# Performance work log

Hardware: AMD Instinct MI355X
Metric: run time of the kernel (lower is better)

## Reference

```python
import jax, jax.numpy as jnp
import numpy as np

N, D = 8192, 256
ALPHA, BETA, K = 50.0, 1.0, 2


def setup_inputs() -> dict:
    key = jax.random.key(0)
    k1, k2, k3, k4 = jax.random.split(key, 4)
    Q = jax.random.normal(k1, (N, D), dtype=jnp.float32)
    # 0/1 similarity structure; diagonal forced nonzero so no row is fully masked
    sim = jax.random.randint(k2, (N, N), 0, 2).astype(jnp.float32)
    sim = sim.at[jnp.arange(N), jnp.arange(N)].set(1.0)
    # nn.Linear(in_dim, in_dim) params: y = x @ W.T + b
    bound = 1.0 / np.sqrt(D)
    W = jax.random.uniform(k3, (D, D), jnp.float32, -bound, bound)
    b = jax.random.uniform(k4, (D,), jnp.float32, -bound, bound)
    return {"Q": Q, "sim_mat": sim, "W": W, "b": b}


def reference(Q, sim_mat, W, b):
    mask = sim_mat == 0  # (N, N) bool, constant across iterations
    H = Q
    for _ in range(K):
        H_proj = H @ W.T + b                      # (N, d)
        scores = H_proj @ H_proj.T                # (N, N)
        scores = jnp.where(mask, -jnp.inf, scores)
        lamb = jax.nn.softmax(scores, axis=1)     # (N, N)
        numerator = ALPHA * Q + BETA * (lamb @ H)
        denominator = ALPHA + BETA * jnp.sum(lamb, axis=1, keepdims=True)
        H = numerator / denominator
    return H
```

## Files before the change

### kernel.cpp

```cpp
#include <hip/hip_runtime.h>
#include <hip/hip_bf16.h>

#define NN 8192
#define DD 256
#define ALPHA 50.0f
#define BETA 1.0f
#define THR 10.0f
#define KQ 8
#define KEYS (NN / KQ)
#define KTILE 64
#define ITERS (KEYS / KTILE)
#define QROWS 128

typedef __attribute__((ext_vector_type(8))) short short8;
typedef __attribute__((ext_vector_type(4))) float f32x4;

static __device__ __forceinline__ ushort f2bf(float f) {
    union { __hip_bfloat16 h; ushort u; } v;
    v.h = __float2bfloat16(f);
    return v.u;
}
static __device__ __forceinline__ float bf2f(ushort u) {
    union { unsigned u; float f; } v; v.u = ((unsigned)u) << 16;
    return v.f;
}
static __device__ __forceinline__ void gl_lds16(const void* g, void* l) {
    __builtin_amdgcn_global_load_lds(
        (const __attribute__((address_space(1))) unsigned int*)g,
        (__attribute__((address_space(3))) unsigned int*)l, 16, 0, 0);
}

__global__ void k_wconv(const float* __restrict__ W, ushort* __restrict__ Wb) {
    int i = blockIdx.x * 256 + threadIdx.x;
    Wb[i] = f2bf(W[i]);
}

__global__ __launch_bounds__(256) void k_pack(const float* __restrict__ sim,
                                              unsigned* __restrict__ bits) {
    __shared__ unsigned char nibs[256];
    int row = blockIdx.x;
    int tid = threadIdx.x;
    for (int p = 0; p < 8; ++p) {
        int col = p * 1024 + tid * 4;
        float4 v = *reinterpret_cast<const float4*>(sim + (size_t)row * NN + col);
        unsigned char nib = (unsigned char)((v.x != 0.f) | ((v.y != 0.f) << 1) |
                                            ((v.z != 0.f) << 2) | ((v.w != 0.f) << 3));
        nibs[tid] = nib;
        __syncthreads();
        if (tid < 32) {
            unsigned word = 0;
#pragma unroll
            for (int i = 0; i < 8; ++i) word |= ((unsigned)nibs[tid * 8 + i]) << (4 * i);
            bits[row * (NN / 32) + p * 32 + tid] = word;
        }
        __syncthreads();
    }
}

__global__ __launch_bounds__(256) void k_convert(const float* __restrict__ H,
                                                 ushort* __restrict__ Hv,
                                                 ushort* __restrict__ Hvt) {
    __shared__ ushort T[64][72];
    int tile = blockIdx.x;
    int r0 = (tile >> 2) * 64;
    int c0 = (tile & 3) * 64;
    int tid = threadIdx.x;
    int tr = tid >> 4;
    int tc = (tid & 15) * 4;
    for (int i = 0; i < 4; ++i) {
        int r = tr + i * 16;
        float4 v = *reinterpret_cast<const float4*>(H + (size_t)(r0 + r) * DD + c0 + tc);
        ushort4 o;
        o.x = f2bf(v.x); o.y = f2bf(v.y); o.z = f2bf(v.z); o.w = f2bf(v.w);
        *reinterpret_cast<ushort4*>(Hv + (size_t)(r0 + r) * DD + c0 + tc) = o;
        T[tc + 0][r] = o.x; T[tc + 1][r] = o.y; T[tc + 2][r] = o.z; T[tc + 3][r] = o.w;
    }
    __syncthreads();
    for (int i = 0; i < 4; ++i) {
        int c = tr + i * 16;
        ushort4 o;
        o.x = T[c][tc + 0]; o.y = T[c][tc + 1]; o.z = T[c][tc + 2]; o.w = T[c][tc + 3];
        *reinterpret_cast<ushort4*>(Hvt + (size_t)(c0 + c) * NN + r0 + tc) = o;
    }
}

__global__ __launch_bounds__(256) void k_proj(const ushort* __restrict__ Hv,
                                              const ushort* __restrict__ Wb,
                                              const float* __restrict__ b,
                                              ushort* __restrict__ Hp) {
    int w = threadIdx.x >> 6;
    int lane = threadIdx.x & 63;
    int row0 = (blockIdx.x >> 1) * 64 + w * 16;
    int ch = blockIdx.x & 1;
    int lr = lane & 15;
    int lk = lane >> 4;
    short8 af[8];
    for (int kk = 0; kk < 8; ++kk)
        af[kk] = *reinterpret_cast<const short8*>(Hv + (size_t)(row0 + lr) * DD + kk * 32 + lk * 8);
    for (int t = 0; t < 8; ++t) {
        f32x4 acc = {0.f, 0.f, 0.f, 0.f};
        int col = (ch * 8 + t) * 16 + lr;
        for (int kk = 0; kk < 8; ++kk) {
            short8 bf = *reinterpret_cast<const short8*>(Wb + (size_t)col * DD + kk * 32 + lk * 8);
            acc = __builtin_amdgcn_mfma_f32_16x16x32_bf16(af[kk], bf, acc, 0, 0, 0);
        }
        float bias = b[col];
        for (int j = 0; j < 4; ++j) {
            int row = row0 + lk * 4 + j;
            Hp[(size_t)row * DD + col] = f2bf(acc[j] + bias);
        }
    }
}

#define PSTR 40
#define KBYTES (KTILE * 256 * 2)
#define VBYTES (256 * KTILE * 2)
#define PBYTES (8 * 16 * PSTR * 2)
#define BBYTES (QROWS * 32 * 4)
#define SMEM_ATTN (2 * KBYTES + 2 * VBYTES + PBYTES + BBYTES)
__global__ __launch_bounds__(512) void k_attn(const ushort* __restrict__ Hp,
                                              const ushort* __restrict__ Hvt,
                                              const unsigned* __restrict__ bits,
                                              ushort* __restrict__ Opart,
                                              float* __restrict__ mpart,
                                              float* __restrict__ lpart) {
    extern __shared__ char smem[];
    ushort* KlB = (ushort*)smem;
    ushort* VlB = (ushort*)(smem + 2 * KBYTES);
    ushort* Pl  = (ushort*)(smem + 2 * KBYTES + 2 * VBYTES);
    unsigned* Bl = (unsigned*)(smem + 2 * KBYTES + 2 * VBYTES + PBYTES);

    const int tid = threadIdx.x;
    const int w = tid >> 6;
    const int lane = tid & 63;
    const int lr = lane & 15;
    const int lk = lane >> 4;
    const int bid = blockIdx.x;
    const int kq = bid & 7;
    const int qt = bid >> 3;
    const int rw0 = qt * QROWS + w * 16;
    const int kstart = kq * KEYS;

    int kSrc[4], vSrc[4], dstO[4];
#pragma unroll
    for (int i = 0; i < 4; ++i) {
        int S = i * 512 + tid;
        int rK = S >> 5, cpK = S & 31;
        kSrc[i] = rK * 256 + (cpK ^ (rK & 7)) * 8;
        int rV = S >> 3, cpV = S & 7;
        vSrc[i] = rV * NN + (cpV ^ (rV & 7)) * 8;
        dstO[i] = S * 8;
    }
    auto stageK = [&](int buf, int kb) {
        const ushort* Kg = Hp + (size_t)kb * DD;
        ushort* base = KlB + buf * (KTILE * 256);
#pragma unroll
        for (int i = 0; i < 4; ++i) gl_lds16(Kg + kSrc[i], base + dstO[i]);
    };
    auto stageV = [&](int buf, int kb) {
        const ushort* Vg = Hvt + kb;
        ushort* base = VlB + buf * (256 * KTILE);
#pragma unroll
        for (int i = 0; i < 4; ++i) gl_lds16(Vg + vSrc[i], base + dstO[i]);
    };

    int Koff[8];
#pragma unroll
    for (int kk = 0; kk < 8; ++kk)
        Koff[kk] = (lr << 9) + ((((kk << 2) + lk) ^ (lr & 7)) << 4);
    const int vBaseA = (lr << 7) + ((lk ^ (lr & 7)) << 4);
    const int vBaseB = (lr << 7) + (((4 + lk) ^ (lr & 7)) << 4);

    short8 qf[8];
#pragma unroll
    for (int kk = 0; kk < 8; ++kk)
        qf[kk] = *reinterpret_cast<const short8*>(Hp + (size_t)(rw0 + lr) * DD + kk * 32 + lk * 8);

    f32x4 o[17];
#pragma unroll
    for (int t = 0; t < 17; ++t) o[t] = {0.f, 0.f, 0.f, 0.f};
    float m[4] = {-1e30f, -1e30f, -1e30f, -1e30f};

    short8 ones;
#pragma unroll
    for (int e = 0; e < 8; ++e) ones[e] = (short)0x3f80;

    {
        const unsigned* Bg = bits + (size_t)(qt * QROWS) * (NN / 32) + kq * 32;
#pragma unroll
        for (int i = 0; i < 2; ++i) {
            int S = i * 512 + tid;
            int r = S >> 3, c = S & 7;
            gl_lds16(Bg + (size_t)r * (NN / 32) + c * 4, Bl + S * 4);
        }
    }
    stageK(0, kstart);
    stageV(0, kstart);
    asm volatile("s_waitcnt vmcnt(0)" ::: "memory");
    __builtin_amdgcn_s_barrier();
    __builtin_amdgcn_sched_barrier(0);

    ushort* Pw = Pl + (size_t)w * 16 * PSTR;
    const int mrow = (w * 16 + lk * 4) * 32;
    int cur = 0;
    for (int it = 0; it < ITERS; ++it) {
        const int kb = kstart + it * KTILE;
        const bool staged = (it + 1 < ITERS);
        if (staged) {
            stageK(cur ^ 1, kb + KTILE);
            stageV(cur ^ 1, kb + KTILE);
        }
        unsigned mwa[4], mwb[4];
#pragma unroll
        for (int j = 0; j < 4; ++j) {
            mwa[j] = Bl[mrow + j * 32 + it * 2];
            mwb[j] = Bl[mrow + j * 32 + it * 2 + 1];
        }

        const char* Kb = (const char*)(KlB + cur * (KTILE * 256));
        f32x4 s0a = {0.f,0.f,0.f,0.f}, s1a = {0.f,0.f,0.f,0.f};
        f32x4 s0b = {0.f,0.f,0.f,0.f}, s1b = {0.f,0.f,0.f,0.f};
        __builtin_amdgcn_s_setprio(1);
#pragma unroll
        for (int kk = 0; kk < 8; ++kk) {
            short8 k0a = *reinterpret_cast<const short8*>(Kb + Koff[kk]);
            short8 k1a = *reinterpret_cast<const short8*>(Kb + Koff[kk] + (16 << 9));
            short8 k0b = *reinterpret_cast<const short8*>(Kb + Koff[kk] + (32 << 9));
            short8 k1b = *reinterpret_cast<const short8*>(Kb + Koff[kk] + (48 << 9));
            s0a = __builtin_amdgcn_mfma_f32_16x16x32_bf16(qf[kk], k0a, s0a, 0, 0, 0);
            s1a = __builtin_amdgcn_mfma_f32_16x16x32_bf16(qf[kk], k1a, s1a, 0, 0, 0);
            s0b = __builtin_amdgcn_mfma_f32_16x16x32_bf16(qf[kk], k0b, s0b, 0, 0, 0);
            s1b = __builtin_amdgcn_mfma_f32_16x16x32_bf16(qf[kk], k1b, s1b, 0, 0, 0);
        }
        __builtin_amdgcn_s_setprio(0);

        const char* Vb = (const char*)(VlB + cur * (256 * KTILE));
        {
            float c = -1e30f;
#pragma unroll
            for (int j = 0; j < 4; ++j) {
                float a0 = ((mwa[j] >> lr) & 1u) ? s0a[j] : -1e30f;
                float a1 = ((mwa[j] >> (lr + 16)) & 1u) ? s1a[j] : -1e30f;
                s0a[j] = a0; s1a[j] = a1;
                c = fmaxf(c, fmaxf(a0, a1) - m[j]);
            }
            if (__any(c > THR)) {
#pragma unroll
                for (int j = 0; j < 4; ++j) {
                    float mx = fmaxf(s0a[j], s1a[j]);
                    mx = fmaxf(mx, __shfl_xor(mx, 1));
                    mx = fmaxf(mx, __shfl_xor(mx, 2));
                    mx = fmaxf(mx, __shfl_xor(mx, 4));
                    mx = fmaxf(mx, __shfl_xor(mx, 8));
                    float mn = fmaxf(m[j], mx);
                    float scale = __expf(m[j] - mn);
                    m[j] = mn;
#pragma unroll
                    for (int t = 0; t < 17; ++t) o[t][j] *= scale;
                }
            }
#pragma unroll
            for (int j = 0; j < 4; ++j) {
                Pw[(lk * 4 + j) * PSTR + lr]      = f2bf(__expf(s0a[j] - m[j]));
                Pw[(lk * 4 + j) * PSTR + 16 + lr] = f2bf(__expf(s1a[j] - m[j]));
            }
            asm volatile("s_waitcnt lgkmcnt(0)" ::: "memory");
            __builtin_amdgcn_sched_barrier(0);
            short8 pa = *reinterpret_cast<const short8*>(Pw + lr * PSTR + lk * 8);
            __builtin_amdgcn_s_setprio(1);
#pragma unroll
            for (int t = 0; t < 16; ++t) {
                short8 vf = *reinterpret_cast<const short8*>(Vb + vBaseA + (t << 11));
                o[t] = __builtin_amdgcn_mfma_f32_16x16x32_bf16(pa, vf, o[t], 0, 0, 0);
            }
            o[16] = __builtin_amdgcn_mfma_f32_16x16x32_bf16(pa, ones, o[16], 0, 0, 0);
            __builtin_amdgcn_s_setprio(0);
        }
        {
            float c = -1e30f;
#pragma unroll
            for (int j = 0; j < 4; ++j) {
                float a0 = ((mwb[j] >> lr) & 1u) ? s0b[j] : -1e30f;
                float a1 = ((mwb[j] >> (lr + 16)) & 1u) ? s1b[j] : -1e30f;
                s0b[j] = a0; s1b[j] = a1;
                c = fmaxf(c, fmaxf(a0, a1) - m[j]);
            }
            if (__any(c > THR)) {
#pragma unroll
                for (int j = 0; j < 4; ++j) {
                    float mx = fmaxf(s0b[j], s1b[j]);
                    mx = fmaxf(mx, __shfl_xor(mx, 1));
                    mx = fmaxf(mx, __shfl_xor(mx, 2));
                    mx = fmaxf(mx, __shfl_xor(mx, 4));
                    mx = fmaxf(mx, __shfl_xor(mx, 8));
                    float mn = fmaxf(m[j], mx);
                    float scale = __expf(m[j] - mn);
                    m[j] = mn;
#pragma unroll
                    for (int t = 0; t < 17; ++t) o[t][j] *= scale;
                }
            }
#pragma unroll
            for (int j = 0; j < 4; ++j) {
                Pw[(lk * 4 + j) * PSTR + lr]      = f2bf(__expf(s0b[j] - m[j]));
                Pw[(lk * 4 + j) * PSTR + 16 + lr] = f2bf(__expf(s1b[j] - m[j]));
            }
            asm volatile("s_waitcnt lgkmcnt(0)" ::: "memory");
            __builtin_amdgcn_sched_barrier(0);
            short8 pb = *reinterpret_cast<const short8*>(Pw + lr * PSTR + lk * 8);
            __builtin_amdgcn_s_setprio(1);
#pragma unroll
            for (int t = 0; t < 16; ++t) {
                short8 vf = *reinterpret_cast<const short8*>(Vb + vBaseB + (t << 11));
                o[t] = __builtin_amdgcn_mfma_f32_16x16x32_bf16(pb, vf, o[t], 0, 0, 0);
            }
            o[16] = __builtin_amdgcn_mfma_f32_16x16x32_bf16(pb, ones, o[16], 0, 0, 0);
            __builtin_amdgcn_s_setprio(0);
        }
        if (staged) {
            asm volatile("s_waitcnt vmcnt(0)" ::: "memory");
            __builtin_amdgcn_s_barrier();
            __builtin_amdgcn_sched_barrier(0);
        }
        cur ^= 1;
    }

    ushort* op = Opart + ((size_t)kq * NN + rw0) * DD;
#pragma unroll
    for (int t = 0; t < 16; ++t)
#pragma unroll
        for (int j = 0; j < 4; ++j)
            op[(size_t)(lk * 4 + j) * DD + t * 16 + lr] = f2bf(o[t][j]);
    if (lr == 0) {
#pragma unroll
        for (int j = 0; j < 4; ++j) {
            mpart[kq * NN + rw0 + lk * 4 + j] = m[j];
            lpart[kq * NN + rw0 + lk * 4 + j] = o[16][j];
        }
    }
}

__global__ __launch_bounds__(256) void k_merge8(const ushort* __restrict__ Opart,
                                                const float* __restrict__ mpart,
                                                const float* __restrict__ lpart,
                                                const float* __restrict__ Qo,
                                                float* __restrict__ dst) {
    int w = threadIdx.x >> 6;
    int lane = threadIdx.x & 63;
    int r0 = blockIdx.x * 32 + w * 8;
    for (int rr = 0; rr < 8; ++rr) {
        int r = r0 + rr;
        float mv[8], f[8];
        float M = -1e30f;
#pragma unroll
        for (int p = 0; p < 8; ++p) { mv[p] = mpart[p * NN + r]; M = fmaxf(M, mv[p]); }
        float L = 0.f;
#pragma unroll
        for (int p = 0; p < 8; ++p) { f[p] = __expf(mv[p] - M); L += f[p] * lpart[p * NN + r]; }
        float invL = 1.0f / L;
        int c = lane * 4;
        float a0 = 0.f, a1 = 0.f, a2 = 0.f, a3 = 0.f;
#pragma unroll
        for (int p = 0; p < 8; ++p) {
            ushort4 u = *reinterpret_cast<const ushort4*>(Opart + ((size_t)p * NN + r) * DD + c);
            a0 += f[p] * bf2f(u.x); a1 += f[p] * bf2f(u.y);
            a2 += f[p] * bf2f(u.z); a3 += f[p] * bf2f(u.w);
        }
        float4 qv = *reinterpret_cast<const float4*>(Qo + (size_t)r * DD + c);
        float4 ov;
        ov.x = (ALPHA * qv.x + a0 * invL) * (1.0f / (ALPHA + BETA));
        ov.y = (ALPHA * qv.y + a1 * invL) * (1.0f / (ALPHA + BETA));
        ov.z = (ALPHA * qv.z + a2 * invL) * (1.0f / (ALPHA + BETA));
        ov.w = (ALPHA * qv.w + a3 * invL) * (1.0f / (ALPHA + BETA));
        *reinterpret_cast<float4*>(dst + (size_t)r * DD + c) = ov;
    }
}

extern "C" void kernel_launch(void* const* d_in, const int* in_sizes, int n_in,
                              void* d_out, int out_size, void* d_ws, size_t ws_size,
                              hipStream_t stream) {
    const float* Q   = (const float*)d_in[0];
    const float* sim = (const float*)d_in[1];
    const float* W   = (const float*)d_in[2];
    const float* b   = (const float*)d_in[3];
    float* out = (float*)d_out;

    char* ws = (char*)d_ws;
    size_t off = 0;
    ushort* Hv   = (ushort*)(ws + off); off += (size_t)NN * DD * 2;
    ushort* HvtA = (ushort*)(ws + off); off += (size_t)NN * DD * 2;
    ushort* HvtB = (ushort*)(ws + off); off += (size_t)NN * DD * 2;
    ushort* Hp   = (ushort*)(ws + off); off += (size_t)NN * DD * 2;
    ushort* Wb   = (ushort*)(ws + off); off += (size_t)DD * DD * 2;
    unsigned* bits = (unsigned*)(ws + off); off += (size_t)NN * (NN / 32) * 4;
    float*  H1   = (float*)(ws + off);  off += (size_t)NN * DD * 4;
    ushort* Opart = (ushort*)(ws + off); off += (size_t)KQ * NN * DD * 2;
    float*  mpart = (float*)(ws + off);  off += (size_t)KQ * NN * 4;
    float*  lpart = (float*)(ws + off);  off += (size_t)KQ * NN * 4;

    (void)hipFuncSetAttribute((const void*)k_attn,
                              hipFuncAttributeMaxDynamicSharedMemorySize, SMEM_ATTN);

    k_wconv<<<DD * DD / 256, 256, 0, stream>>>(W, Wb);
    k_pack<<<NN, 256, 0, stream>>>(sim, bits);
    k_convert<<<(NN / 64) * (DD / 64), 256, 0, stream>>>(Q, Hv, HvtA);

    k_proj<<<NN / 32, 256, 0, stream>>>(Hv, Wb, b, Hp);
    k_attn<<<(NN / QROWS) * KQ, 512, SMEM_ATTN, stream>>>(Hp, HvtA, bits, Opart, mpart, lpart);
    k_merge8<<<NN / 32, 256, 0, stream>>>(Opart, mpart, lpart, Q, H1);
    k_convert<<<(NN / 64) * (DD / 64), 256, 0, stream>>>(H1, Hv, HvtB);

    k_proj<<<NN / 32, 256, 0, stream>>>(Hv, Wb, b, Hp);
    k_attn<<<(NN / QROWS) * KQ, 512, SMEM_ATTN, stream>>>(Hp, HvtB, bits, Opart, mpart, lpart);
    k_merge8<<<NN / 32, 256, 0, stream>>>(Opart, mpart, lpart, Q, out);
}
```

Baseline: 330.5 us.

## Replace double-buffered K/V staging with single buffer and direct mask reads

Removes the double-buffered K/V LDS staging and the LDS copy of the mask bitwords. Each iteration now finishes its compute, hits a barrier, loads the next K/V tile and waits for it, and mask bits are read straight from global memory. This cuts LDS use, which could let more blocks fit per CU, but it gives up overlap between loads and MFMA work and adds a barrier per iteration.

```diff
diff --git a/kernel.cpp b/kernel.cpp
--- a/kernel.cpp
+++ b/kernel.cpp
@@ -116,8 +116,7 @@
 #define KBYTES (KTILE * 256 * 2)
 #define VBYTES (256 * KTILE * 2)
 #define PBYTES (8 * 16 * PSTR * 2)
-#define BBYTES (QROWS * 32 * 4)
-#define SMEM_ATTN (2 * KBYTES + 2 * VBYTES + PBYTES + BBYTES)
+#define SMEM_ATTN (KBYTES + VBYTES + PBYTES)
 __global__ __launch_bounds__(512) void k_attn(const ushort* __restrict__ Hp,
                                               const ushort* __restrict__ Hvt,
                                               const unsigned* __restrict__ bits,
@@ -125,10 +124,9 @@
                                               float* __restrict__ mpart,
                                               float* __restrict__ lpart) {
     extern __shared__ char smem[];
-    ushort* KlB = (ushort*)smem;
-    ushort* VlB = (ushort*)(smem + 2 * KBYTES);
-    ushort* Pl  = (ushort*)(smem + 2 * KBYTES + 2 * VBYTES);
-    unsigned* Bl = (unsigned*)(smem + 2 * KBYTES + 2 * VBYTES + PBYTES);
+    ushort* Kl = (ushort*)smem;
+    ushort* Vl = (ushort*)(smem + KBYTES);
+    ushort* Pl = (ushort*)(smem + KBYTES + VBYTES);
 
     const int tid = threadIdx.x;
     const int w = tid >> 6;
@@ -151,17 +149,15 @@
         vSrc[i] = rV * NN + (cpV ^ (rV & 7)) * 8;
         dstO[i] = S * 8;
     }
-    auto stageK = [&](int buf, int kb) {
+    auto stageK = [&](int kb) {
         const ushort* Kg = Hp + (size_t)kb * DD;
-        ushort* base = KlB + buf * (KTILE * 256);
-#pragma unroll
-        for (int i = 0; i < 4; ++i) gl_lds16(Kg + kSrc[i], base + dstO[i]);
+#pragma unroll
+        for (int i = 0; i < 4; ++i) gl_lds16(Kg + kSrc[i], Kl + dstO[i]);
     };
-    auto stageV = [&](int buf, int kb) {
+    auto stageV = [&](int kb) {
         const ushort* Vg = Hvt + kb;
-        ushort* base = VlB + buf * (256 * KTILE);
-#pragma unroll
-        for (int i = 0; i < 4; ++i) gl_lds16(Vg + vSrc[i], base + dstO[i]);
+#pragma unroll
+        for (int i = 0; i < 4; ++i) gl_lds16(Vg + vSrc[i], Vl + dstO[i]);
     };
 
     int Koff[8];
@@ -185,39 +181,25 @@
 #pragma unroll
     for (int e = 0; e < 8; ++e) ones[e] = (short)0x3f80;
 
-    {
-        const unsigned* Bg = bits + (size_t)(qt * QROWS) * (NN / 32) + kq * 32;
-#pragma unroll
-        for (int i = 0; i < 2; ++i) {
-            int S = i * 512 + tid;
-            int r = S >> 3, c = S & 7;
-            gl_lds16(Bg + (size_t)r * (NN / 32) + c * 4, Bl + S * 4);
-        }
-    }
-    stageK(0, kstart);
-    stageV(0, kstart);
+    stageK(kstart);
+    stageV(kstart);
     asm volatile("s_waitcnt vmcnt(0)" ::: "memory");
     __builtin_amdgcn_s_barrier();
     __builtin_amdgcn_sched_barrier(0);
 
     ushort* Pw = Pl + (size_t)w * 16 * PSTR;
-    const int mrow = (w * 16 + lk * 4) * 32;
-    int cur = 0;
+    const int rowbase = (rw0 + lk * 4) * (NN / 32);
     for (int it = 0; it < ITERS; ++it) {
         const int kb = kstart + it * KTILE;
-        const bool staged = (it + 1 < ITERS);
-        if (staged) {
-            stageK(cur ^ 1, kb + KTILE);
-            stageV(cur ^ 1, kb + KTILE);
-        }
+        const int wi = kb >> 5;
         unsigned mwa[4], mwb[4];
 #pragma unroll
         for (int j = 0; j < 4; ++j) {
-            mwa[j] = Bl[mrow + j * 32 + it * 2];
-            mwb[j] = Bl[mrow + j * 32 + it * 2 + 1];
-        }
-
-        const char* Kb = (const char*)(KlB + cur * (KTILE * 256));
+            mwa[j] = bits[rowbase + j * (NN / 32) + wi];
+            mwb[j] = bits[rowbase + j * (NN / 32) + wi + 1];
+        }
+
+        const char* Kb = (const char*)Kl;
         f32x4 s0a = {0.f,0.f,0.f,0.f}, s1a = {0.f,0.f,0.f,0.f};
         f32x4 s0b = {0.f,0.f,0.f,0.f}, s1b = {0.f,0.f,0.f,0.f};
         __builtin_amdgcn_s_setprio(1);
@@ -234,7 +216,7 @@
         }
         __builtin_amdgcn_s_setprio(0);
 
-        const char* Vb = (const char*)(VlB + cur * (256 * KTILE));
+        const char* Vb = (const char*)Vl;
         {
             float c = -1e30f;
 #pragma unroll
@@ -317,12 +299,15 @@
             o[16] = __builtin_amdgcn_mfma_f32_16x16x32_bf16(pb, ones, o[16], 0, 0, 0);
             __builtin_amdgcn_s_setprio(0);
         }
-        if (staged) {
+        if (it + 1 < ITERS) {
+            __builtin_amdgcn_s_barrier();
+            __builtin_amdgcn_sched_barrier(0);
+            stageK(kb + KTILE);
+            stageV(kb + KTILE);
             asm volatile("s_waitcnt vmcnt(0)" ::: "memory");
             __builtin_amdgcn_s_barrier();
             __builtin_amdgcn_sched_barrier(0);
         }
-        cur ^= 1;
     }
 
     ushort* op = Opart + ((size_t)kq * NN + rw0) * DD;
```

Measured after the change: 342.1 us. +3.5%, slower.

## Process two 16-row query tiles per wave to reuse K/V LDS fragments

Applied to the files above, without the earlier changes.

Each wave now handles 32 query rows (two 16-row sub-tiles) instead of 16, doubling the block's query tile to 256 rows. Every K and V fragment read from LDS feeds two MFMAs, halving LDS read traffic per unit of work and halving how often K/V tiles are staged from global memory. The mask bitmap is no longer preloaded into LDS and is read directly from global memory each iteration. In exchange, register pressure roughly doubles (two sets of 17 accumulators plus Q fragments), which risks spilling or lower occupancy, and the grid now has half as many blocks.

```diff
diff --git a/kernel.cpp b/kernel.cpp
--- a/kernel.cpp
+++ b/kernel.cpp
@@ -10,7 +10,7 @@
 #define KEYS (NN / KQ)
 #define KTILE 64
 #define ITERS (KEYS / KTILE)
-#define QROWS 128
+#define QROWS 256
 
 typedef __attribute__((ext_vector_type(8))) short short8;
 typedef __attribute__((ext_vector_type(4))) float f32x4;
@@ -115,9 +115,8 @@
 #define PSTR 40
 #define KBYTES (KTILE * 256 * 2)
 #define VBYTES (256 * KTILE * 2)
-#define PBYTES (8 * 16 * PSTR * 2)
-#define BBYTES (QROWS * 32 * 4)
-#define SMEM_ATTN (2 * KBYTES + 2 * VBYTES + PBYTES + BBYTES)
+#define PBYTES (8 * 2 * 16 * PSTR * 2)
+#define SMEM_ATTN (2 * KBYTES + 2 * VBYTES + PBYTES)
 __global__ __launch_bounds__(512) void k_attn(const ushort* __restrict__ Hp,
                                               const ushort* __restrict__ Hvt,
                                               const unsigned* __restrict__ bits,
@@ -128,7 +127,6 @@
     ushort* KlB = (ushort*)smem;
     ushort* VlB = (ushort*)(smem + 2 * KBYTES);
     ushort* Pl  = (ushort*)(smem + 2 * KBYTES + 2 * VBYTES);
-    unsigned* Bl = (unsigned*)(smem + 2 * KBYTES + 2 * VBYTES + PBYTES);
 
     const int tid = threadIdx.x;
     const int w = tid >> 6;
@@ -138,7 +136,7 @@
     const int bid = blockIdx.x;
     const int kq = bid & 7;
     const int qt = bid >> 3;
-    const int rw0 = qt * QROWS + w * 16;
+    const int rw0 = qt * QROWS + w * 32;
     const int kstart = kq * KEYS;
 
     int kSrc[4], vSrc[4], dstO[4];
@@ -171,55 +169,55 @@
     const int vBaseA = (lr << 7) + ((lk ^ (lr & 7)) << 4);
     const int vBaseB = (lr << 7) + (((4 + lk) ^ (lr & 7)) << 4);
 
-    short8 qf[8];
-#pragma unroll
-    for (int kk = 0; kk < 8; ++kk)
-        qf[kk] = *reinterpret_cast<const short8*>(Hp + (size_t)(rw0 + lr) * DD + kk * 32 + lk * 8);
-
-    f32x4 o[17];
-#pragma unroll
-    for (int t = 0; t < 17; ++t) o[t] = {0.f, 0.f, 0.f, 0.f};
-    float m[4] = {-1e30f, -1e30f, -1e30f, -1e30f};
+    short8 qfA[8], qfB[8];
+#pragma unroll
+    for (int kk = 0; kk < 8; ++kk) {
+        qfA[kk] = *reinterpret_cast<const short8*>(Hp + (size_t)(rw0 + lr) * DD + kk * 32 + lk * 8);
+        qfB[kk] = *reinterpret_cast<const short8*>(Hp + (size_t)(rw0 + 16 + lr) * DD + kk * 32 + lk * 8);
+    }
+
+    f32x4 oA[17], oB[17];
+#pragma unroll
+    for (int t = 0; t < 17; ++t) { oA[t] = {0.f,0.f,0.f,0.f}; oB[t] = {0.f,0.f,0.f,0.f}; }
+    float mA[4] = {-1e30f, -1e30f, -1e30f, -1e30f};
+    float mB[4] = {-1e30f, -1e30f, -1e30f, -1e30f};
 
     short8 ones;
 #pragma unroll
     for (int e = 0; e < 8; ++e) ones[e] = (short)0x3f80;
 
-    {
-        const unsigned* Bg = bits + (size_t)(qt * QROWS) * (NN / 32) + kq * 32;
-#pragma unroll
-        for (int i = 0; i < 2; ++i) {
-            int S = i * 512 + tid;
-            int r = S >> 3, c = S & 7;
-            gl_lds16(Bg + (size_t)r * (NN / 32) + c * 4, Bl + S * 4);
-        }
-    }
     stageK(0, kstart);
     stageV(0, kstart);
     asm volatile("s_waitcnt vmcnt(0)" ::: "memory");
     __builtin_amdgcn_s_barrier();
     __builtin_amdgcn_sched_barrier(0);
 
-    ushort* Pw = Pl + (size_t)w * 16 * PSTR;
-    const int mrow = (w * 16 + lk * 4) * 32;
+    ushort* PwA = Pl + (size_t)(w * 2) * 16 * PSTR;
+    ushort* PwB = PwA + 16 * PSTR;
+    const int rbA = (rw0 + lk * 4) * (NN / 32);
+    const int rbB = rbA + 16 * (NN / 32);
     int cur = 0;
     for (int it = 0; it < ITERS; ++it) {
         const int kb = kstart + it * KTILE;
-        const bool staged = (it + 1 < ITERS);
-        if (staged) {
+        if (it + 1 < ITERS) {
             stageK(cur ^ 1, kb + KTILE);
             stageV(cur ^ 1, kb + KTILE);
         }
-        unsigned mwa[4], mwb[4];
+        const int wi = kb >> 5;
+        unsigned mAa[4], mAb[4], mBa[4], mBb[4];
 #pragma unroll
         for (int j = 0; j < 4; ++j) {
-            mwa[j] = Bl[mrow + j * 32 + it * 2];
-            mwb[j] = Bl[mrow + j * 32 + it * 2 + 1];
+            mAa[j] = bits[rbA + j * (NN / 32) + wi];
+            mAb[j] = bits[rbA + j * (NN / 32) + wi + 1];
+            mBa[j] = bits[rbB + j * (NN / 32) + wi];
+            mBb[j] = bits[rbB + j * (NN / 32) + wi + 1];
         }
 
         const char* Kb = (const char*)(KlB + cur * (KTILE * 256));
-        f32x4 s0a = {0.f,0.f,0.f,0.f}, s1a = {0.f,0.f,0.f,0.f};
-        f32x4 s0b = {0.f,0.f,0.f,0.f}, s1b = {0.f,0.f,0.f,0.f};
+        f32x4 sA0a = {0.f,0.f,0.f,0.f}, sA1a = {0.f,0.f,0.f,0.f};
+        f32x4 sA0b = {0.f,0.f,0.f,0.f}, sA1b = {0.f,0.f,0.f,0.f};
+        f32x4 sB0a = {0.f,0.f,0.f,0.f}, sB1a = {0.f,0.f,0.f,0.f};
+        f32x4 sB0b = {0.f,0.f,0.f,0.f}, sB1b = {0.f,0.f,0.f,0.f};
         __builtin_amdgcn_s_setprio(1);
 #pragma unroll
         for (int kk = 0; kk < 8; ++kk) {
@@ -227,10 +225,14 @@
             short8 k1a = *reinterpret_cast<const short8*>(Kb + Koff[kk] + (16 << 9));
             short8 k0b = *reinterpret_cast<const short8*>(Kb + Koff[kk] + (32 << 9));
             short8 k1b = *reinterpret_cast<const short8*>(Kb + Koff[kk] + (48 << 9));
-            s0a = __builtin_amdgcn_mfma_f32_16x16x32_bf16(qf[kk], k0a, s0a, 0, 0, 0);
-            s1a = __builtin_amdgcn_mfma_f32_16x16x32_bf16(qf[kk], k1a, s1a, 0, 0, 0);
-            s0b = __builtin_amdgcn_mfma_f32_16x16x32_bf16(qf[kk], k0b, s0b, 0, 0, 0);
-            s1b = __builtin_amdgcn_mfma_f32_16x16x32_bf16(qf[kk], k1b, s1b, 0, 0, 0);
+            sA0a = __builtin_amdgcn_mfma_f32_16x16x32_bf16(qfA[kk], k0a, sA0a, 0, 0, 0);
+            sB0a = __builtin_amdgcn_mfma_f32_16x16x32_bf16(qfB[kk], k0a, sB0a, 0, 0, 0);
+            sA1a = __builtin_amdgcn_mfma_f32_16x16x32_bf16(qfA[kk], k1a, sA1a, 0, 0, 0);
+            sB1a = __builtin_amdgcn_mfma_f32_16x16x32_bf16(qfB[kk], k1a, sB1a, 0, 0, 0);
+            sA0b = __builtin_amdgcn_mfma_f32_16x16x32_bf16(qfA[kk], k0b, sA0b, 0, 0, 0);
+            sB0b = __builtin_amdgcn_mfma_f32_16x16x32_bf16(qfB[kk], k0b, sB0b, 0, 0, 0);
+            sA1b = __builtin_amdgcn_mfma_f32_16x16x32_bf16(qfA[kk], k1b, sA1b, 0, 0, 0);
+            sB1b = __builtin_amdgcn_mfma_f32_16x16x32_bf16(qfB[kk], k1b, sB1b, 0, 0, 0);
         }
         __builtin_amdgcn_s_setprio(0);
 
@@ -239,85 +241,123 @@
             float c = -1e30f;
 #pragma unroll
             for (int j = 0; j < 4; ++j) {
-                float a0 = ((mwa[j] >> lr) & 1u) ? s0a[j] : -1e30f;
-                float a1 = ((mwa[j] >> (lr + 16)) & 1u) ? s1a[j] : -1e30f;
-                s0a[j] = a0; s1a[j] = a1;
-                c = fmaxf(c, fmaxf(a0, a1) - m[j]);
+                float x0 = ((mAa[j] >> lr) & 1u) ? sA0a[j] : -1e30f;
+                float x1 = ((mAa[j] >> (lr + 16)) & 1u) ? sA1a[j] : -1e30f;
+                sA0a[j] = x0; sA1a[j] = x1;
+                c = fmaxf(c, fmaxf(x0, x1) - mA[j]);
+                float y0 = ((mBa[j] >> lr) & 1u) ? sB0a[j] : -1e30f;
+                float y1 = ((mBa[j] >> (lr + 16)) & 1u) ? sB1a[j] : -1e30f;
+                sB0a[j] = y0; sB1a[j] = y1;
+                c = fmaxf(c, fmaxf(y0, y1) - mB[j]);
             }
             if (__any(c > THR)) {
 #pragma unroll
                 for (int j = 0; j < 4; ++j) {
-                    float mx = fmaxf(s0a[j], s1a[j]);
+                    float mx = fmaxf(sA0a[j], sA1a[j]);
                     mx = fmaxf(mx, __shfl_xor(mx, 1));
                     mx = fmaxf(mx, __shfl_xor(mx, 2));
                     mx = fmaxf(mx, __shfl_xor(mx, 4));
                     mx = fmaxf(mx, __shfl_xor(mx, 8));
-                    float mn = fmaxf(m[j], mx);
-                    float scale = __expf(m[j] - mn);
-                    m[j] = mn;
-#pragma unroll
-                    for (int t = 0; t < 17; ++t) o[t][j] *= scale;
+                    float mn = fmaxf(mA[j], mx);
+                    float sc = __expf(mA[j] - mn);
+                    mA[j] = mn;
+#pragma unroll
+                    for (int t = 0; t < 17; ++t) oA[t][j] *= sc;
+                    float my = fmaxf(sB0a[j], sB1a[j]);
+                    my = fmaxf(my, __shfl_xor(my, 1));
+                    my = fmaxf(my, __shfl_xor(my, 2));
+                    my = fmaxf(my, __shfl_xor(my, 4));
+                    my = fmaxf(my, __shfl_xor(my, 8));
+                    float mn2 = fmaxf(mB[j], my);
+                    float sc2 = __expf(mB[j] - mn2);
+                    mB[j] = mn2;
+#pragma unroll
+                    for (int t = 0; t < 17; ++t) oB[t][j] *= sc2;
                 }
             }
 #pragma unroll
             for (int j = 0; j < 4; ++j) {
-                Pw[(lk * 4 + j) * PSTR + lr]      = f2bf(__expf(s0a[j] - m[j]));
-                Pw[(lk * 4 + j) * PSTR + 16 + lr] = f2bf(__expf(s1a[j] - m[j]));
+                PwA[(lk * 4 + j) * PSTR + lr]      = f2bf(__expf(sA0a[j] - mA[j]));
+                PwA[(lk * 4 + j) * PSTR + 16 + lr] = f2bf(__expf(sA1a[j] - mA[j]));
+                PwB[(lk * 4 + j) * PSTR + lr]      = f2bf(__expf(sB0a[j] - mB[j]));
+                PwB[(lk * 4 + j) * PSTR + 16 + lr] = f2bf(__expf(sB1a[j] - mB[j]));
             }
             asm volatile("s_waitcnt lgkmcnt(0)" ::: "memory");
             __builtin_amdgcn_sched_barrier(0);
-            short8 pa = *reinterpret_cast<const short8*>(Pw + lr * PSTR + lk * 8);
+            short8 paA = *reinterpret_cast<const short8*>(PwA + lr * PSTR + lk * 8);
+            short8 paB = *reinterpret_cast<const short8*>(PwB + lr * PSTR + lk * 8);
             __builtin_amdgcn_s_setprio(1);
 #pragma unroll
             for (int t = 0; t < 16; ++t) {
                 short8 vf = *reinterpret_cast<const short8*>(Vb + vBaseA + (t << 11));
-                o[t] = __builtin_amdgcn_mfma_f32_16x16x32_bf16(pa, vf, o[t], 0, 0, 0);
-            }
-            o[16] = __builtin_amdgcn_mfma_f32_16x16x32_bf16(pa, ones, o[16], 0, 0, 0);
+                oA[t] = __builtin_amdgcn_mfma_f32_16x16x32_bf16(paA, vf, oA[t], 0, 0, 0);
+                oB[t] = __builtin_amdgcn_mfma_f32_16x16x32_bf16(paB, vf, oB[t], 0, 0, 0);
+            }
+            oA[16] = __builtin_amdgcn_mfma_f32_16x16x32_bf16(paA, ones, oA[16], 0, 0, 0);
+            oB[16] = __builtin_amdgcn_mfma_f32_16x16x32_bf16(paB, ones, oB[16], 0, 0, 0);
             __builtin_amdgcn_s_setprio(0);
         }
         {
             float c = -1e30f;
 #pragma unroll
             for (int j = 0; j < 4; ++j) {
-                float a0 = ((mwb[j] >> lr) & 1u) ? s0b[j] : -1e30f;
-                float a1 = ((mwb[j] >> (lr + 16)) & 1u) ? s1b[j] : -1e30f;
-                s0b[j] = a0; s1b[j] = a1;
-                c = fmaxf(c, fmaxf(a0, a1) - m[j]);
+                float x0 = ((mAb[j] >> lr) & 1u) ? sA0b[j] : -1e30f;
+                float x1 = ((mAb[j] >> (lr + 16)) & 1u) ? sA1b[j] : -1e30f;
+                sA0b[j] = x0; sA1b[j] = x1;
+                c = fmaxf(c, fmaxf(x0, x1) - mA[j]);
+                float y0 = ((mBb[j] >> lr) & 1u) ? sB0b[j] : -1e30f;
+                float y1 = ((mBb[j] >> (lr + 16)) & 1u) ? sB1b[j] : -1e30f;
+                sB0b[j] = y0; sB1b[j] = y1;
+                c = fmaxf(c, fmaxf(y0, y1) - mB[j]);
             }
             if (__any(c > THR)) {
 #pragma unroll
                 for (int j = 0; j < 4; ++j) {
-                    float mx = fmaxf(s0b[j], s1b[j]);
+                    float mx = fmaxf(sA0b[j], sA1b[j]);
                     mx = fmaxf(mx, __shfl_xor(mx, 1));
                     mx = fmaxf(mx, __shfl_xor(mx, 2));
                     mx = fmaxf(mx, __shfl_xor(mx, 4));
                     mx = fmaxf(mx, __shfl_xor(mx, 8));
-                    float mn = fmaxf(m[j], mx);
-                    float scale = __expf(m[j] - mn);
-                    m[j] = mn;
-#pragma unroll
-                    for (int t = 0; t < 17; ++t) o[t][j] *= scale;
+                    float mn = fmaxf(mA[j], mx);
+                    float sc = __expf(mA[j] - mn);
+                    mA[j] = mn;
+#pragma unroll
+                    for (int t = 0; t < 17; ++t) oA[t][j] *= sc;
+                    float my = fmaxf(sB0b[j], sB1b[j]);
+                    my = fmaxf(my, __shfl_xor(my, 1));
+                    my = fmaxf(my, __shfl_xor(my, 2));
+                    my = fmaxf(my, __shfl_xor(my, 4));
+                    my = fmaxf(my, __shfl_xor(my, 8));
+                    float mn2 = fmaxf(mB[j], my);
+                    float sc2 = __expf(mB[j] - mn2);
+                    mB[j] = mn2;
+#pragma unroll
+                    for (int t = 0; t < 17; ++t) oB[t][j] *= sc2;
                 }
             }
 #pragma unroll
             for (int j = 0; j < 4; ++j) {
-                Pw[(lk * 4 + j) * PSTR + lr]      = f2bf(__expf(s0b[j] - m[j]));
-                Pw[(lk * 4 + j) * PSTR + 16 + lr] = f2bf(__expf(s1b[j] - m[j]));
+                PwA[(lk * 4 + j) * PSTR + lr]      = f2bf(__expf(sA0b[j] - mA[j]));
+                PwA[(lk * 4 + j) * PSTR + 16 + lr] = f2bf(__expf(sA1b[j] - mA[j]));
+                PwB[(lk * 4 + j) * PSTR + lr]      = f2bf(__expf(sB0b[j] - mB[j]));
+                PwB[(lk * 4 + j) * PSTR + 16 + lr] = f2bf(__expf(sB1b[j] - mB[j]));
             }
             asm volatile("s_waitcnt lgkmcnt(0)" ::: "memory");
             __builtin_amdgcn_sched_barrier(0);
-            short8 pb = *reinterpret_cast<const short8*>(Pw + lr * PSTR + lk * 8);
+            short8 paA = *reinterpret_cast<const short8*>(PwA + lr * PSTR + lk * 8);
+            short8 paB = *reinterpret_cast<const short8*>(PwB + lr * PSTR + lk * 8);
             __builtin_amdgcn_s_setprio(1);
 #pragma unroll
             for (int t = 0; t < 16; ++t) {
                 short8 vf = *reinterpret_cast<const short8*>(Vb + vBaseB + (t << 11));
-                o[t] = __builtin_amdgcn_mfma_f32_16x16x32_bf16(pb, vf, o[t], 0, 0, 0);
-            }
-            o[16] = __builtin_amdgcn_mfma_f32_16x16x32_bf16(pb, ones, o[16], 0, 0, 0);
+                oA[t] = __builtin_amdgcn_mfma_f32_16x16x32_bf16(paA, vf, oA[t], 0, 0, 0);
+                oB[t] = __builtin_amdgcn_mfma_f32_16x16x32_bf16(paB, vf, oB[t], 0, 0, 0);
+            }
+            oA[16] = __builtin_amdgcn_mfma_f32_16x16x32_bf16(paA, ones, oA[16], 0, 0, 0);
+            oB[16] = __builtin_amdgcn_mfma_f32_16x16x32_bf16(paB, ones, oB[16], 0, 0, 0);
             __builtin_amdgcn_s_setprio(0);
         }
-        if (staged) {
+        if (it + 1 < ITERS) {
             asm volatile("s_waitcnt vmcnt(0)" ::: "memory");
             __builtin_amdgcn_s_barrier();
             __builtin_amdgcn_sched_barrier(0);
@@ -325,17 +365,22 @@
         cur ^= 1;
     }
 
-    ushort* op = Opart + ((size_t)kq * NN + rw0) * DD;
+    ushort* opA = Opart + ((size_t)kq * NN + rw0) * DD;
+    ushort* opB = opA + (size_t)16 * DD;
 #pragma unroll
     for (int t = 0; t < 16; ++t)
 #pragma unroll
-        for (int j = 0; j < 4; ++j)
-            op[(size_t)(lk * 4 + j) * DD + t * 16 + lr] = f2bf(o[t][j]);
+        for (int j = 0; j < 4; ++j) {
+            opA[(size_t)(lk * 4 + j) * DD + t * 16 + lr] = f2bf(oA[t][j]);
+            opB[(size_t)(lk * 4 + j) * DD + t * 16 + lr] = f2bf(oB[t][j]);
+        }
     if (lr == 0) {
 #pragma unroll
         for (int j = 0; j < 4; ++j) {
-            mpart[kq * NN + rw0 + lk * 4 + j] = m[j];
-            lpart[kq * NN + rw0 + lk * 4 + j] = o[16][j];
+            mpart[kq * NN + rw0 + lk * 4 + j] = mA[j];
+            lpart[kq * NN + rw0 + lk * 4 + j] = oA[16][j];
+            mpart[kq * NN + rw0 + 16 + lk * 4 + j] = mB[j];
+            lpart[kq * NN + rw0 + 16 + lk * 4 + j] = oB[16][j];
         }
     }
 }
```

New measurement: 814.7 us. +146.5%, slower.

## Halve key split, read mask bits directly, fuse merge with bf16 convert/transpose

Applied to the files above, without the earlier changes.

Reduces the key-dimension split from 8 to 4 partitions, so each attention block processes twice as many key tiles and the merge combines fewer partials. The LDS staging of mask bits is dropped and each wave reads bit words straight from global memory every iteration. The merge kernel now also emits the bf16 row-major and transposed copies of H for the next iteration, which removes the separate fp32 H1 buffer and the convert kernel. The cost is a smaller grid (fewer blocks to fill CUs), longer per-block loops, and extra global loads of mask words inside the inner loop.

```diff
diff --git a/kernel.cpp b/kernel.cpp
--- a/kernel.cpp
+++ b/kernel.cpp
@@ -6,7 +6,7 @@
 #define ALPHA 50.0f
 #define BETA 1.0f
 #define THR 10.0f
-#define KQ 8
+#define KQ 4
 #define KEYS (NN / KQ)
 #define KTILE 64
 #define ITERS (KEYS / KTILE)
@@ -116,8 +116,7 @@
 #define KBYTES (KTILE * 256 * 2)
 #define VBYTES (256 * KTILE * 2)
 #define PBYTES (8 * 16 * PSTR * 2)
-#define BBYTES (QROWS * 32 * 4)
-#define SMEM_ATTN (2 * KBYTES + 2 * VBYTES + PBYTES + BBYTES)
+#define SMEM_ATTN (2 * KBYTES + 2 * VBYTES + PBYTES)
 __global__ __launch_bounds__(512) void k_attn(const ushort* __restrict__ Hp,
                                               const ushort* __restrict__ Hvt,
                                               const unsigned* __restrict__ bits,
@@ -128,7 +127,6 @@
     ushort* KlB = (ushort*)smem;
     ushort* VlB = (ushort*)(smem + 2 * KBYTES);
     ushort* Pl  = (ushort*)(smem + 2 * KBYTES + 2 * VBYTES);
-    unsigned* Bl = (unsigned*)(smem + 2 * KBYTES + 2 * VBYTES + PBYTES);
 
     const int tid = threadIdx.x;
     const int w = tid >> 6;
@@ -136,8 +134,8 @@
     const int lr = lane & 15;
     const int lk = lane >> 4;
     const int bid = blockIdx.x;
-    const int kq = bid & 7;
-    const int qt = bid >> 3;
+    const int kq = bid & 3;
+    const int qt = bid >> 2;
     const int rw0 = qt * QROWS + w * 16;
     const int kstart = kq * KEYS;
 
@@ -185,15 +183,6 @@
 #pragma unroll
     for (int e = 0; e < 8; ++e) ones[e] = (short)0x3f80;
 
-    {
-        const unsigned* Bg = bits + (size_t)(qt * QROWS) * (NN / 32) + kq * 32;
-#pragma unroll
-        for (int i = 0; i < 2; ++i) {
-            int S = i * 512 + tid;
-            int r = S >> 3, c = S & 7;
-            gl_lds16(Bg + (size_t)r * (NN / 32) + c * 4, Bl + S * 4);
-        }
-    }
     stageK(0, kstart);
     stageV(0, kstart);
     asm volatile("s_waitcnt vmcnt(0)" ::: "memory");
@@ -201,7 +190,7 @@
     __builtin_amdgcn_sched_barrier(0);
 
     ushort* Pw = Pl + (size_t)w * 16 * PSTR;
-    const int mrow = (w * 16 + lk * 4) * 32;
+    const int rowbase = (rw0 + lk * 4) * (NN / 32);
     int cur = 0;
     for (int it = 0; it < ITERS; ++it) {
         const int kb = kstart + it * KTILE;
@@ -210,11 +199,12 @@
             stageK(cur ^ 1, kb + KTILE);
             stageV(cur ^ 1, kb + KTILE);
         }
+        const int wi = kb >> 5;
         unsigned mwa[4], mwb[4];
 #pragma unroll
         for (int j = 0; j < 4; ++j) {
-            mwa[j] = Bl[mrow + j * 32 + it * 2];
-            mwb[j] = Bl[mrow + j * 32 + it * 2 + 1];
+            mwa[j] = bits[rowbase + j * (NN / 32) + wi];
+            mwb[j] = bits[rowbase + j * (NN / 32) + wi + 1];
         }
 
         const char* Kb = (const char*)(KlB + cur * (KTILE * 256));
@@ -340,28 +330,31 @@
     }
 }
 
-__global__ __launch_bounds__(256) void k_merge8(const ushort* __restrict__ Opart,
+__global__ __launch_bounds__(256) void k_merge4(const ushort* __restrict__ Opart,
                                                 const float* __restrict__ mpart,
                                                 const float* __restrict__ lpart,
                                                 const float* __restrict__ Qo,
-                                                float* __restrict__ dst) {
+                                                float* __restrict__ dst,
+                                                ushort* __restrict__ HvOut,
+                                                ushort* __restrict__ HvtOut) {
+    __shared__ ushort T[32][264];
     int w = threadIdx.x >> 6;
     int lane = threadIdx.x & 63;
     int r0 = blockIdx.x * 32 + w * 8;
     for (int rr = 0; rr < 8; ++rr) {
         int r = r0 + rr;
-        float mv[8], f[8];
+        float mv[KQ], f[KQ];
         float M = -1e30f;
 #pragma unroll
-        for (int p = 0; p < 8; ++p) { mv[p] = mpart[p * NN + r]; M = fmaxf(M, mv[p]); }
+        for (int p = 0; p < KQ; ++p) { mv[p] = mpart[p * NN + r]; M = fmaxf(M, mv[p]); }
         float L = 0.f;
 #pragma unroll
-        for (int p = 0; p < 8; ++p) { f[p] = __expf(mv[p] - M); L += f[p] * lpart[p * NN + r]; }
+        for (int p = 0; p < KQ; ++p) { f[p] = __expf(mv[p] - M); L += f[p] * lpart[p * NN + r]; }
         float invL = 1.0f / L;
         int c = lane * 4;
         float a0 = 0.f, a1 = 0.f, a2 = 0.f, a3 = 0.f;
 #pragma unroll
-        for (int p = 0; p < 8; ++p) {
+        for (int p = 0; p < KQ; ++p) {
             ushort4 u = *reinterpret_cast<const ushort4*>(Opart + ((size_t)p * NN + r) * DD + c);
             a0 += f[p] * bf2f(u.x); a1 += f[p] * bf2f(u.y);
             a2 += f[p] * bf2f(u.z); a3 += f[p] * bf2f(u.w);
@@ -372,7 +365,27 @@
         ov.y = (ALPHA * qv.y + a1 * invL) * (1.0f / (ALPHA + BETA));
         ov.z = (ALPHA * qv.z + a2 * invL) * (1.0f / (ALPHA + BETA));
         ov.w = (ALPHA * qv.w + a3 * invL) * (1.0f / (ALPHA + BETA));
-        *reinterpret_cast<float4*>(dst + (size_t)r * DD + c) = ov;
+        if (dst) *reinterpret_cast<float4*>(dst + (size_t)r * DD + c) = ov;
+        ushort4 bv;
+        bv.x = f2bf(ov.x); bv.y = f2bf(ov.y); bv.z = f2bf(ov.z); bv.w = f2bf(ov.w);
+        if (HvOut) *reinterpret_cast<ushort4*>(HvOut + (size_t)r * DD + c) = bv;
+        if (HvtOut) {
+            int rl = w * 8 + rr;
+            T[rl][c] = bv.x; T[rl][c + 1] = bv.y; T[rl][c + 2] = bv.z; T[rl][c + 3] = bv.w;
+        }
+    }
+    if (HvtOut) {
+        __syncthreads();
+        int col = threadIdx.x;
+        int R0 = blockIdx.x * 32;
+        ushort* dstp = HvtOut + (size_t)col * NN + R0;
+#pragma unroll
+        for (int k = 0; k < 8; ++k) {
+            ushort4 u;
+            u.x = T[k * 4 + 0][col]; u.y = T[k * 4 + 1][col];
+            u.z = T[k * 4 + 2][col]; u.w = T[k * 4 + 3][col];
+            *reinterpret_cast<ushort4*>(dstp + k * 4) = u;
+        }
     }
 }
 
@@ -393,7 +406,6 @@
     ushort* Hp   = (ushort*)(ws + off); off += (size_t)NN * DD * 2;
     ushort* Wb   = (ushort*)(ws + off); off += (size_t)DD * DD * 2;
     unsigned* bits = (unsigned*)(ws + off); off += (size_t)NN * (NN / 32) * 4;
-    float*  H1   = (float*)(ws + off);  off += (size_t)NN * DD * 4;
     ushort* Opart = (ushort*)(ws + off); off += (size_t)KQ * NN * DD * 2;
     float*  mpart = (float*)(ws + off);  off += (size_t)KQ * NN * 4;
     float*  lpart = (float*)(ws + off);  off += (size_t)KQ * NN * 4;
@@ -407,10 +419,9 @@
 
     k_proj<<<NN / 32, 256, 0, stream>>>(Hv, Wb, b, Hp);
     k_attn<<<(NN / QROWS) * KQ, 512, SMEM_ATTN, stream>>>(Hp, HvtA, bits, Opart, mpart, lpart);
-    k_merge8<<<NN / 32, 256, 0, stream>>>(Opart, mpart, lpart, Q, H1);
-    k_convert<<<(NN / 64) * (DD / 64), 256, 0, stream>>>(H1, Hv, HvtB);
+    k_merge4<<<NN / 32, 256, 0, stream>>>(Opart, mpart, lpart, Q, nullptr, Hv, HvtB);
 
     k_proj<<<NN / 32, 256, 0, stream>>>(Hv, Wb, b, Hp);
     k_attn<<<(NN / QROWS) * KQ, 512, SMEM_ATTN, stream>>>(Hp, HvtB, bits, Opart, mpart, lpart);
-    k_merge8<<<NN / 32, 256, 0, stream>>>(Opart, mpart, lpart, Q, out);
-}
+    k_merge4<<<NN / 32, 256, 0, stream>>>(Opart, mpart, lpart, Q, out, nullptr, nullptr);
+}
```

Result: faster. 298.5 us (median of 2 runs) (-9.7%).
